# Performance work log

Hardware: AMD Instinct MI355X
Metric: run time of the kernel (lower is better)

The kernel has to match this reference:

```python
import jax, jax.numpy as jnp
import numpy as np

BSZ, SEQ, HID = 4, 2048, 2048
NH, NKV, HD = 16, 8, 128
SLOTS, MAXSEQ = 8, 4096
EPS = 1e-6
SCALE = HD ** -0.5


def rms_norm(x, w):
    # normalize over last dim (head_dim)
    var = jnp.mean(jnp.square(x), axis=-1, keepdims=True)
    return x * jax.lax.rsqrt(var + EPS) * w


def setup_inputs() -> dict:
    key = jax.random.key(0)
    ks = jax.random.split(key, 6)
    return {
        "hidden_states": jax.random.normal(ks[0], (BSZ, SEQ, HID), jnp.float32),
        "positions": jnp.tile(jnp.arange(SEQ, dtype=jnp.int32)[None, :], (BSZ, 1)),
        "k_cache": jnp.zeros((SLOTS, MAXSEQ, NKV, HD), jnp.float32),
        "v_cache": jnp.zeros((SLOTS, MAXSEQ, NKV, HD), jnp.float32),
        "slot_mapping": jnp.arange(BSZ, dtype=jnp.int32),
        "kv_start_indices": jnp.zeros((BSZ,), jnp.int32),
        "seq_lens": jnp.full((BSZ,), SEQ, jnp.int32),
        "qkv_w": jax.random.normal(ks[1], ((NH + 2 * NKV) * HD, HID), jnp.float32) * 0.02,
        "qkv_b": jax.random.normal(ks[2], ((NH + 2 * NKV) * HD,), jnp.float32) * 0.02,
        "o_w": jax.random.normal(ks[3], (HID, NH * HD), jnp.float32) * 0.02,
        "q_norm_w": jnp.ones((HD,), jnp.float32),
        "k_norm_w": jnp.ones((HD,), jnp.float32),
    }


def reference(hidden_states, positions, k_cache, v_cache, slot_mapping,
              kv_start_indices, seq_lens, qkv_w, qkv_b, o_w, q_norm_w, k_norm_w):
    bsz, seq_len, _ = hidden_states.shape
    qkv = jnp.einsum("bsh,oh->bso", hidden_states, qkv_w) + qkv_b
    q, k, v = jnp.split(qkv, [NH * HD, NH * HD + NKV * HD], axis=-1)
    q = rms_norm(q.reshape(bsz, seq_len, NH, HD), q_norm_w)
    k = rms_norm(k.reshape(bsz, seq_len, NKV, HD), k_norm_w)
    v = v.reshape(bsz, seq_len, NKV, HD)

    # paged KV cache scatter: cache[slot, start:start+seq] = k/v  (vectorized over batch)
    rows = kv_start_indices[:, None] + jnp.arange(seq_len)[None, :]  # [B,S]
    k_cache = k_cache.at[slot_mapping[:, None], rows].set(k)
    v_cache = v_cache.at[slot_mapping[:, None], rows].set(v)

    # prefill path (seq_len > 1): gather back up to max_l (= seq_len here, static)
    max_l = seq_len
    k_h = k_cache[slot_mapping, :max_l].transpose(0, 2, 1, 3)  # [B,Hkv,L,D]
    v_h = v_cache[slot_mapping, :max_l].transpose(0, 2, 1, 3)
    n_rep = NH // NKV
    if n_rep > 1:  # repeat_interleave over head dim (GQA)
        k_h = jnp.repeat(k_h, n_rep, axis=1)
        v_h = jnp.repeat(v_h, n_rep, axis=1)

    qh = q.transpose(0, 2, 1, 3)  # [B,H,S,D]
    scores = jnp.einsum("bhqd,bhkd->bhqk", qh, k_h) * SCALE
    causal = jnp.tril(jnp.ones((seq_len, max_l), bool))
    scores = jnp.where(causal[None, None], scores, -jnp.inf)
    attn = jax.nn.softmax(scores, axis=-1)
    out = jnp.einsum("bhqk,bhkd->bhqd", attn, v_h)
    out = out.transpose(0, 2, 1, 3).reshape(bsz, seq_len, NH * HD)
    return jnp.einsum("bso,ho->bsh", out, o_w)
```

## Files before the change

### kernel.cpp

```cpp
#include <hip/hip_runtime.h>
#include <hip/hip_bf16.h>
#include <stdint.h>

typedef unsigned short u16;
typedef __attribute__((ext_vector_type(8))) __bf16 bf16x8;
typedef __attribute__((ext_vector_type(4))) float f32x4;

#define EPSF 1e-6f
#define SCALE 0.08838834764831845f

__device__ __forceinline__ u16 f2bf(float f) {
    union { float f; uint32_t u; } a; a.f = f;
    uint32_t r = a.u + 0x7FFFu + ((a.u >> 16) & 1u);
    return (u16)(r >> 16);
}
__device__ __forceinline__ float bf2f(u16 u) {
    union { uint32_t u; float f; } a; a.u = ((uint32_t)u) << 16;
    return a.f;
}
__device__ __forceinline__ u16 f2bf_n(float f) {
    __hip_bfloat16 h = __float2bfloat16(f);
    return *reinterpret_cast<u16*>(&h);
}

__global__ __launch_bounds__(256) void cvt_all_k(
    const float* __restrict__ a,
    const float* __restrict__ b,
    const float* __restrict__ c,
    u16* __restrict__ out)
{
    long i = (long)blockIdx.x * 256 + threadIdx.x;
    const float* src; long off;
    if (i < 4194304L)      { src = a; off = 0; }
    else if (i < 6291456L) { src = b; off = 4194304L; }
    else                   { src = c; off = 6291456L; }
    float4 v = ((const float4*)src)[i - off];
    ushort4 o;
    o.x = f2bf(v.x); o.y = f2bf(v.y); o.z = f2bf(v.z); o.w = f2bf(v.w);
    ((ushort4*)out)[i] = o;
}

__device__ __forceinline__ void gload16(const u16* g, u16* l) {
    __builtin_amdgcn_global_load_lds(
        (const __attribute__((address_space(1))) uint32_t*)g,
        (__attribute__((address_space(3))) uint32_t*)l, 16, 0, 0);
}

__global__ __launch_bounds__(512, 2) void gemm8_nt(
    const u16* __restrict__ A, const u16* __restrict__ B,
    const float* __restrict__ bias,
    float* __restrict__ Cf, u16* __restrict__ Cb,
    int M, int N, int K)
{
    __shared__ u16 As[2][256 * 64];
    __shared__ u16 Bs[2][256 * 64];

    const int t = threadIdx.x;
    const int lane = t & 63;
    const int g = lane >> 4, lr = lane & 15;
    const int w = t >> 6;
    const int wm = w >> 2, wn = w & 3;

    const int nwg = gridDim.x * gridDim.y;
    const int bid0 = blockIdx.y * gridDim.x + blockIdx.x;
    const int cpx = nwg >> 3;
    const int bids = (bid0 & 7) * cpx + (bid0 >> 3);
    const int bn = (bids % gridDim.x) * 256;
    const int bm = (bids / gridDim.x) * 256;
    const int NT = K >> 6;

    f32x4 z = {0.f, 0.f, 0.f, 0.f};
    f32x4 acc[8][4];
#pragma unroll
    for (int m = 0; m < 8; ++m)
#pragma unroll
        for (int n = 0; n < 4; ++n) acc[m][n] = z;

    auto STAGE2 = [&](int buf, int k0, int p) {
#pragma unroll
        for (int j = 0; j < 2; ++j) {
            int idx = p * 1024 + j * 512 + t;
            int ci = idx & 2047;
            int row = ci >> 3, slot = ci & 7;
            int csrc = slot ^ (row & 7);
            if (idx < 2048)
                gload16(A + (size_t)(bm + row) * K + k0 + csrc * 8, &As[buf][0] + ci * 8);
            else
                gload16(B + (size_t)(bn + row) * K + k0 + csrc * 8, &Bs[buf][0] + ci * 8);
        }
    };

    bf16x8 afr0[4][2], afr1[4][2];
    bf16x8 bf0[2][2], bf1[2][2];

#pragma unroll
    for (int p = 0; p < 4; ++p) STAGE2(0, 0, p);

    for (int kt = 0; kt < NT; ++kt) {
        const int cur = kt & 1;
        const int k0n = (kt + 1) << 6;
        const bool last = (kt == NT - 1);
        const char* Ab = (const char*)&As[cur][0];
        const char* Bb = (const char*)&Bs[cur][0];
        const int swz = (lr & 7) << 4;

        auto LDA = [&](bf16x8 (&dst)[4][2], int mbase) {
#pragma unroll
            for (int mi = 0; mi < 4; ++mi) {
                int row = wm * 128 + (mbase + mi) * 16 + lr;
#pragma unroll
                for (int kc = 0; kc < 2; ++kc)
                    dst[mi][kc] = *(const bf16x8*)(Ab + row * 128 + ((kc * 64 + g * 16) ^ swz));
            }
        };
        auto LDB = [&](bf16x8 (&dst)[2][2], int nbase) {
#pragma unroll
            for (int ni = 0; ni < 2; ++ni) {
                int row = wn * 64 + (nbase + ni) * 16 + lr;
#pragma unroll
                for (int kc = 0; kc < 2; ++kc)
                    dst[ni][kc] = *(const bf16x8*)(Bb + row * 128 + ((kc * 64 + g * 16) ^ swz));
            }
        };
        auto MMA = [&](bf16x8 (&amf)[4][2], int mf0, int nf0, bf16x8 (&bfr)[2][2]) {
            __builtin_amdgcn_s_setprio(1);
#pragma unroll
            for (int mi = 0; mi < 4; ++mi)
#pragma unroll
                for (int ni = 0; ni < 2; ++ni)
#pragma unroll
                    for (int kc = 0; kc < 2; ++kc)
                        acc[mf0 + mi][nf0 + ni] = __builtin_amdgcn_mfma_f32_16x16x32_bf16(
                            amf[mi][kc], bfr[ni][kc], acc[mf0 + mi][nf0 + ni], 0, 0, 0);
            __builtin_amdgcn_s_setprio(0);
        };

        if (!last) {
#pragma unroll
            for (int p = 0; p < 4; ++p) STAGE2(cur ^ 1, k0n, p);
            asm volatile("s_waitcnt vmcnt(8)" ::: "memory");
        } else {
            asm volatile("s_waitcnt vmcnt(0)" ::: "memory");
        }
        __builtin_amdgcn_s_barrier();
        __builtin_amdgcn_sched_barrier(0);

        LDA(afr0, 0); LDB(bf0, 0); LDB(bf1, 2);
        MMA(afr0, 0, 0, bf0);
        MMA(afr0, 0, 2, bf1);
        LDA(afr1, 4);
        MMA(afr1, 4, 2, bf1);
        MMA(afr1, 4, 0, bf0);

        __builtin_amdgcn_sched_barrier(0);
        __builtin_amdgcn_s_barrier();
    }

#pragma unroll
    for (int mf = 0; mf < 8; ++mf) {
#pragma unroll
        for (int nf = 0; nf < 4; ++nf) {
            int col = bn + wn * 64 + nf * 16 + lr;
            float bv = bias ? bias[col] : 0.f;
#pragma unroll
            for (int r = 0; r < 4; ++r) {
                int row = bm + wm * 128 + mf * 16 + g * 4 + r;
                float v = acc[mf][nf][r] + bv;
                if (Cf) Cf[(size_t)row * N + col] = v;
                else    Cb[(size_t)row * N + col] = f2bf(v);
            }
        }
    }
}

__global__ __launch_bounds__(256) void prep_k(
    u16* __restrict__ qkv, const float* __restrict__ qw, const float* __restrict__ kw,
    u16* __restrict__ vt)
{
    __shared__ u16 T[64 * 64];
    const int bid = blockIdx.x;
    const int t = threadIdx.x;

    if (bid < 8192) {
        const int row = bid;
        const int w = t >> 6, l = t & 63;
#pragma unroll
        for (int i = 0; i < 6; ++i) {
            int head = w + i * 4;
            const float* wt = (head < 16) ? qw : kw;
            u16* p = qkv + (size_t)row * 4096 + head * 128;
            uint32_t u = *(const uint32_t*)(p + l * 2);
            float x0 = bf2f((u16)(u & 0xFFFF));
            float x1 = bf2f((u16)(u >> 16));
            float ss = x0 * x0 + x1 * x1;
#pragma unroll
            for (int m = 1; m < 64; m <<= 1) ss += __shfl_xor(ss, m, 64);
            float inv = rsqrtf(ss * (1.0f / 128.0f) + EPSF);
            float r0 = x0 * inv * wt[l * 2];
            float r1 = x1 * inv * wt[l * 2 + 1];
            uint32_t o = (uint32_t)f2bf(r0) | ((uint32_t)f2bf(r1) << 16);
            *(uint32_t*)(p + l * 2) = o;
        }
    } else {
        const int q = bid - 8192;
        const int sx = (q & 31) * 64;
        const int dy = ((q >> 5) & 1) * 64;
        const int z  = q >> 6;
        const int b = z >> 3, hk = z & 7;
#pragma unroll
        for (int j = 0; j < 2; ++j) {
            int idx = t + j * 256;
            int r = idx >> 3, c8 = (idx & 7) * 8;
            uint4 v = *(const uint4*)(qkv + (size_t)(b * 2048 + sx + r) * 4096 + 3072 + hk * 128 + dy + c8);
            int slot = (c8 >> 3) ^ ((r ^ (r >> 3)) & 7);
            *(uint4*)(&T[r * 64 + slot * 8]) = v;
        }
        __syncthreads();
#pragma unroll
        for (int j = 0; j < 2; ++j) {
            int idx = t + j * 256;
            int rr = idx >> 3, cc8 = (idx & 7) * 8;
            u16 tmp[8];
#pragma unroll
            for (int i = 0; i < 8; ++i) {
                int row = cc8 + i;
                int slot = (rr >> 3) ^ ((row ^ (row >> 3)) & 7);
                tmp[i] = T[row * 64 + slot * 8 + (rr & 7)];
            }
            *(uint4*)(vt + ((size_t)z * 128 + dy + rr) * 2048 + sx + cc8) = *(uint4*)tmp;
        }
    }
}

__global__ __launch_bounds__(256, 2) void attn7_k(
    const u16* __restrict__ qkv, const u16* __restrict__ vt,
    u16* __restrict__ aout)
{
    __shared__ u16 Kt[2][64 * 128];
    __shared__ u16 Vl[2][128 * 64];

    const int t = threadIdx.x;
    const int lane = t & 63;
    const int w = t >> 6;
    const int g = lane >> 4, lr = lane & 15;
    const int pr = blockIdx.x, h = blockIdx.y, b = blockIdx.z;
    const int hk = h >> 1;
    const size_t rowb = (size_t)b * 2048;

    const u16* ksrc = qkv + rowb * 4096 + 2048 + hk * 128;
    const u16* vsrc = vt + (size_t)(b * 8 + hk) * 128 * 2048;

    bf16x8 ones8;
    {
        union { bf16x8 v; u16 e[8]; } on;
#pragma unroll
        for (int j = 0; j < 8; ++j) on.e[j] = 0x3F80;
        ones8 = on.v;
    }

    auto STAGE = [&](int buf, int kvb) {
#pragma unroll
        for (int j = 0; j < 4; ++j) {
            int idx = t + j * 256;
            {
                int row = idx >> 4, slot = idx & 15;
                int csrc = (slot & 8) | ((slot & 7) ^ (row & 7));
                gload16(ksrc + (size_t)(kvb + row) * 4096 + csrc * 8, &Kt[buf][0] + idx * 8);
            }
            {
                int row = idx >> 3, slot = idx & 7;
                int csrc = slot ^ (row & 7);
                gload16(vsrc + (size_t)row * 2048 + kvb + csrc * 8, &Vl[buf][0] + idx * 8);
            }
        }
    };

    for (int sub = 0; sub < 2; ++sub) {
        const int qt = sub ? 15 - pr : pr;
        const int qbase = qt * 128;
        const int nt = 2 * qt + 2;

        bf16x8 qf[2][4];
        {
            const u16* qp = qkv + (rowb + qbase + w * 32 + lr) * 4096 + h * 128;
#pragma unroll
            for (int sb = 0; sb < 2; ++sb)
#pragma unroll
                for (int c = 0; c < 4; ++c) {
                    union { bf16x8 v; u16 e[8]; } uq;
                    uq.v = *(const bf16x8*)(qp + sb * 16 * 4096 + c * 32 + g * 8);
#pragma unroll
                    for (int jj = 0; jj < 8; ++jj) uq.e[jj] = f2bf(bf2f(uq.e[jj]) * SCALE);
                    qf[sb][c] = uq.v;
                }
        }

        float m_r2[2];
        f32x4 z = {0.f, 0.f, 0.f, 0.f};
        f32x4 l_acc[2];
        f32x4 o_acc[2][8];
#pragma unroll
        for (int sb = 0; sb < 2; ++sb) {
            m_r2[sb] = -INFINITY;
            l_acc[sb] = z;
#pragma unroll
            for (int d = 0; d < 8; ++d) o_acc[sb][d] = z;
        }

        __syncthreads();
        STAGE(0, 0);

        for (int kt = 0; kt < nt; ++kt) {
            const int cur = kt & 1;
            const int kvb = kt * 64;
            asm volatile("s_waitcnt vmcnt(0)" ::: "memory");
            __builtin_amdgcn_s_barrier();
            __builtin_amdgcn_sched_barrier(0);
            if (kt + 1 < nt) STAGE(cur ^ 1, kvb + 64);
            __builtin_amdgcn_sched_barrier(0);

            const u16* Kc = &Kt[cur][0];
            const u16* Vc = &Vl[cur][0];
            const bool active = !(kt == nt - 1 && w < 2);
            const bool near = (kt >= nt - 2);

            if (active) {
                f32x4 st[2][4];
                __builtin_amdgcn_s_setprio(1);
#pragma unroll
                for (int cb = 0; cb < 4; ++cb) {
                    int row = cb * 16 + lr;
                    st[0][cb] = z; st[1][cb] = z;
#pragma unroll
                    for (int c = 0; c < 4; ++c) {
                        int chunk = c * 4 + g;
                        int slot = (chunk & 8) | ((chunk & 7) ^ (row & 7));
                        bf16x8 kf = *(const bf16x8*)(&Kc[row * 128 + slot * 8]);
                        st[0][cb] = __builtin_amdgcn_mfma_f32_16x16x32_bf16(kf, qf[0][c], st[0][cb], 0, 0, 0);
                        st[1][cb] = __builtin_amdgcn_mfma_f32_16x16x32_bf16(kf, qf[1][c], st[1][cb], 0, 0, 0);
                    }
                }
                __builtin_amdgcn_s_setprio(0);

                const int slo = ((g & 1) << 5) + lr;
                const int shi = slo + 16;
                const bool ghx = (g >> 1) & 1;

#pragma unroll
                for (int sb = 0; sb < 2; ++sb) {
                    const int qa = qbase + w * 32 + sb * 16 + lr;
                    if (near) {
#pragma unroll
                        for (int cb = 0; cb < 4; ++cb)
#pragma unroll
                            for (int r = 0; r < 4; ++r)
                                if (kvb + cb * 16 + g * 4 + r > qa) st[sb][cb][r] = -INFINITY;
                    }
                    f32x4 m4;
#pragma unroll
                    for (int e = 0; e < 4; ++e)
                        m4[e] = fmaxf(fmaxf(st[sb][0][e], st[sb][1][e]),
                                      fmaxf(st[sb][2][e], st[sb][3][e]));
                    float mx = fmaxf(fmaxf(m4[0], m4[1]), fmaxf(m4[2], m4[3]));
                    mx = fmaxf(mx, __shfl_xor(mx, 16));
                    mx = fmaxf(mx, __shfl_xor(mx, 32));
                    float mold = m_r2[sb];
                    float mbase;
                    if (__all(mx <= mold + 8.0f)) {
                        mbase = mold;
                    } else {
                        float mnew = fmaxf(mold, mx);
                        float alpha = __expf(mold - mnew);
#pragma unroll
                        for (int r = 0; r < 4; ++r) {
                            float ar = __shfl(alpha, (lane & 48) | (g * 4 + r), 64);
                            l_acc[sb][r] *= ar;
#pragma unroll
                            for (int d = 0; d < 8; ++d) o_acc[sb][d][r] *= ar;
                        }
                        m_r2[sb] = mnew;
                        mbase = mnew;
                    }
                    uint2 pk[4];
#pragma unroll
                    for (int cb = 0; cb < 4; ++cb) {
                        float p0 = __expf(st[sb][cb][0] - mbase);
                        float p1 = __expf(st[sb][cb][1] - mbase);
                        float p2 = __expf(st[sb][cb][2] - mbase);
                        float p3 = __expf(st[sb][cb][3] - mbase);
                        pk[cb].x = (uint32_t)f2bf_n(p0) | ((uint32_t)f2bf_n(p1) << 16);
                        pk[cb].y = (uint32_t)f2bf_n(p2) | ((uint32_t)f2bf_n(p3) << 16);
                    }

#pragma unroll
                    for (int kk = 0; kk < 2; ++kk) {
                        uint32_t e0 = (uint32_t)__shfl((int)pk[kk * 2].x, slo, 64);
                        uint32_t e1 = (uint32_t)__shfl((int)pk[kk * 2].y, slo, 64);
                        uint32_t e2 = (uint32_t)__shfl((int)pk[kk * 2].x, shi, 64);
                        uint32_t e3 = (uint32_t)__shfl((int)pk[kk * 2].y, shi, 64);
                        uint32_t o0 = (uint32_t)__shfl((int)pk[kk * 2 + 1].x, slo, 64);
                        uint32_t o1 = (uint32_t)__shfl((int)pk[kk * 2 + 1].y, slo, 64);
                        uint32_t o2 = (uint32_t)__shfl((int)pk[kk * 2 + 1].x, shi, 64);
                        uint32_t o3 = (uint32_t)__shfl((int)pk[kk * 2 + 1].y, shi, 64);
                        union { uint32_t u[4]; bf16x8 v; } pa;
                        pa.u[0] = ghx ? o0 : e0;
                        pa.u[1] = ghx ? o1 : e1;
                        pa.u[2] = ghx ? o2 : e2;
                        pa.u[3] = ghx ? o3 : e3;
                        __builtin_amdgcn_s_setprio(1);
                        l_acc[sb] = __builtin_amdgcn_mfma_f32_16x16x32_bf16(pa.v, ones8, l_acc[sb], 0, 0, 0);
#pragma unroll
                        for (int d = 0; d < 8; ++d) {
                            int row = d * 16 + lr;
                            int slot = (kk * 4 + g) ^ (row & 7);
                            bf16x8 vf = *(const bf16x8*)(&Vc[row * 64 + slot * 8]);
                            o_acc[sb][d] = __builtin_amdgcn_mfma_f32_16x16x32_bf16(pa.v, vf, o_acc[sb][d], 0, 0, 0);
                        }
                        __builtin_amdgcn_s_setprio(0);
                    }
                }
            }
            __builtin_amdgcn_sched_barrier(0);
        }

#pragma unroll
        for (int sb = 0; sb < 2; ++sb) {
            const int qrow0 = qbase + w * 32 + sb * 16 + g * 4;
#pragma unroll
            for (int r = 0; r < 4; ++r) {
                float inv = 1.0f / l_acc[sb][r];
                u16* op = aout + (rowb + qrow0 + r) * 2048 + h * 128;
#pragma unroll
                for (int d = 0; d < 8; ++d)
                    op[d * 16 + lr] = f2bf_n(o_acc[sb][d][r] * inv);
            }
        }
    }
}

extern "C" void kernel_launch(void* const* d_in, const int* in_sizes, int n_in,
                              void* d_out, int out_size, void* d_ws, size_t ws_size,
                              hipStream_t stream)
{
    const float* hidden = (const float*)d_in[0];
    const float* qkv_w = (const float*)d_in[7];
    const float* qkv_b = (const float*)d_in[8];
    const float* o_w   = (const float*)d_in[9];
    const float* q_nw  = (const float*)d_in[10];
    const float* k_nw  = (const float*)d_in[11];

    char* ws = (char*)d_ws;
    u16* hid_bf  = (u16*)ws; ws += (size_t)8192 * 2048 * 2;
    u16* wqkv_bf = (u16*)ws; ws += (size_t)4096 * 2048 * 2;
    u16* ow_bf   = (u16*)ws; ws += (size_t)2048 * 2048 * 2;
    u16* qkv_bf  = (u16*)ws; ws += (size_t)8192 * 4096 * 2;
    u16* attn_bf = (u16*)ws; ws += (size_t)8192 * 2048 * 2;
    u16* vt_bf   = hid_bf;

    cvt_all_k<<<28672, 256, 0, stream>>>(hidden, qkv_w, o_w, hid_bf);

    gemm8_nt<<<dim3(16, 32), 512, 0, stream>>>(hid_bf, wqkv_bf, qkv_b,
                                               nullptr, qkv_bf, 8192, 4096, 2048);
    prep_k<<<dim3(10240), 256, 0, stream>>>(qkv_bf, q_nw, k_nw, vt_bf);
    attn7_k<<<dim3(8, 16, 4), 256, 0, stream>>>(qkv_bf, vt_bf, attn_bf);
    gemm8_nt<<<dim3(8, 32), 512, 0, stream>>>(attn_bf, ow_bf, nullptr,
                                              (float*)d_out, nullptr, 8192, 2048, 2048);
}
```

Measured before the change: 378.1 us.

## Shrink GEMM block tile to 128x128 with four waves per block

Replaces the 256x256, 8-wave GEMM with a 128x128, 4-wave variant that has half the LDS footprint and a simpler load-then-MMA inner loop. Grids grow fourfold, giving more blocks per CU and finer load balance. In exchange, per-tile data reuse drops, so global and LDS traffic per FLOP rise, and the interleaved fragment-load/MMA schedule is lost.

```diff
diff --git a/kernel.cpp b/kernel.cpp
--- a/kernel.cpp
+++ b/kernel.cpp
@@ -46,55 +46,51 @@
         (__attribute__((address_space(3))) uint32_t*)l, 16, 0, 0);
 }
 
-__global__ __launch_bounds__(512, 2) void gemm8_nt(
+__global__ __launch_bounds__(256, 2) void gemm4_nt(
     const u16* __restrict__ A, const u16* __restrict__ B,
     const float* __restrict__ bias,
     float* __restrict__ Cf, u16* __restrict__ Cb,
     int M, int N, int K)
 {
-    __shared__ u16 As[2][256 * 64];
-    __shared__ u16 Bs[2][256 * 64];
+    __shared__ u16 As[2][128 * 64];
+    __shared__ u16 Bs[2][128 * 64];
 
     const int t = threadIdx.x;
     const int lane = t & 63;
     const int g = lane >> 4, lr = lane & 15;
     const int w = t >> 6;
-    const int wm = w >> 2, wn = w & 3;
+    const int wm = w >> 1, wn = w & 1;
 
     const int nwg = gridDim.x * gridDim.y;
     const int bid0 = blockIdx.y * gridDim.x + blockIdx.x;
     const int cpx = nwg >> 3;
     const int bids = (bid0 & 7) * cpx + (bid0 >> 3);
-    const int bn = (bids % gridDim.x) * 256;
-    const int bm = (bids / gridDim.x) * 256;
+    const int bn = (bids % gridDim.x) * 128;
+    const int bm = (bids / gridDim.x) * 128;
     const int NT = K >> 6;
 
     f32x4 z = {0.f, 0.f, 0.f, 0.f};
-    f32x4 acc[8][4];
-#pragma unroll
-    for (int m = 0; m < 8; ++m)
+    f32x4 acc[4][4];
+#pragma unroll
+    for (int m = 0; m < 4; ++m)
 #pragma unroll
         for (int n = 0; n < 4; ++n) acc[m][n] = z;
 
-    auto STAGE2 = [&](int buf, int k0, int p) {
-#pragma unroll
-        for (int j = 0; j < 2; ++j) {
-            int idx = p * 1024 + j * 512 + t;
-            int ci = idx & 2047;
+    auto STAGEALL = [&](int buf, int k0) {
+#pragma unroll
+        for (int j = 0; j < 8; ++j) {
+            int idx = j * 256 + t;
+            int ci = idx & 1023;
             int row = ci >> 3, slot = ci & 7;
             int csrc = slot ^ (row & 7);
-            if (idx < 2048)
+            if (idx < 1024)
                 gload16(A + (size_t)(bm + row) * K + k0 + csrc * 8, &As[buf][0] + ci * 8);
             else
                 gload16(B + (size_t)(bn + row) * K + k0 + csrc * 8, &Bs[buf][0] + ci * 8);
         }
     };
 
-    bf16x8 afr0[4][2], afr1[4][2];
-    bf16x8 bf0[2][2], bf1[2][2];
-
-#pragma unroll
-    for (int p = 0; p < 4; ++p) STAGE2(0, 0, p);
+    STAGEALL(0, 0);
 
     for (int kt = 0; kt < NT; ++kt) {
         const int cur = kt & 1;
@@ -104,40 +100,8 @@
         const char* Bb = (const char*)&Bs[cur][0];
         const int swz = (lr & 7) << 4;
 
-        auto LDA = [&](bf16x8 (&dst)[4][2], int mbase) {
-#pragma unroll
-            for (int mi = 0; mi < 4; ++mi) {
-                int row = wm * 128 + (mbase + mi) * 16 + lr;
-#pragma unroll
-                for (int kc = 0; kc < 2; ++kc)
-                    dst[mi][kc] = *(const bf16x8*)(Ab + row * 128 + ((kc * 64 + g * 16) ^ swz));
-            }
-        };
-        auto LDB = [&](bf16x8 (&dst)[2][2], int nbase) {
-#pragma unroll
-            for (int ni = 0; ni < 2; ++ni) {
-                int row = wn * 64 + (nbase + ni) * 16 + lr;
-#pragma unroll
-                for (int kc = 0; kc < 2; ++kc)
-                    dst[ni][kc] = *(const bf16x8*)(Bb + row * 128 + ((kc * 64 + g * 16) ^ swz));
-            }
-        };
-        auto MMA = [&](bf16x8 (&amf)[4][2], int mf0, int nf0, bf16x8 (&bfr)[2][2]) {
-            __builtin_amdgcn_s_setprio(1);
-#pragma unroll
-            for (int mi = 0; mi < 4; ++mi)
-#pragma unroll
-                for (int ni = 0; ni < 2; ++ni)
-#pragma unroll
-                    for (int kc = 0; kc < 2; ++kc)
-                        acc[mf0 + mi][nf0 + ni] = __builtin_amdgcn_mfma_f32_16x16x32_bf16(
-                            amf[mi][kc], bfr[ni][kc], acc[mf0 + mi][nf0 + ni], 0, 0, 0);
-            __builtin_amdgcn_s_setprio(0);
-        };
-
         if (!last) {
-#pragma unroll
-            for (int p = 0; p < 4; ++p) STAGE2(cur ^ 1, k0n, p);
+            STAGEALL(cur ^ 1, k0n);
             asm volatile("s_waitcnt vmcnt(8)" ::: "memory");
         } else {
             asm volatile("s_waitcnt vmcnt(0)" ::: "memory");
@@ -145,26 +109,45 @@
         __builtin_amdgcn_s_barrier();
         __builtin_amdgcn_sched_barrier(0);
 
-        LDA(afr0, 0); LDB(bf0, 0); LDB(bf1, 2);
-        MMA(afr0, 0, 0, bf0);
-        MMA(afr0, 0, 2, bf1);
-        LDA(afr1, 4);
-        MMA(afr1, 4, 2, bf1);
-        MMA(afr1, 4, 0, bf0);
+        bf16x8 afr[4][2], bfr[4][2];
+#pragma unroll
+        for (int mi = 0; mi < 4; ++mi) {
+            int row = wm * 64 + mi * 16 + lr;
+#pragma unroll
+            for (int kc = 0; kc < 2; ++kc)
+                afr[mi][kc] = *(const bf16x8*)(Ab + row * 128 + ((kc * 64 + g * 16) ^ swz));
+        }
+#pragma unroll
+        for (int ni = 0; ni < 4; ++ni) {
+            int row = wn * 64 + ni * 16 + lr;
+#pragma unroll
+            for (int kc = 0; kc < 2; ++kc)
+                bfr[ni][kc] = *(const bf16x8*)(Bb + row * 128 + ((kc * 64 + g * 16) ^ swz));
+        }
+        __builtin_amdgcn_s_setprio(1);
+#pragma unroll
+        for (int mi = 0; mi < 4; ++mi)
+#pragma unroll
+            for (int ni = 0; ni < 4; ++ni)
+#pragma unroll
+                for (int kc = 0; kc < 2; ++kc)
+                    acc[mi][ni] = __builtin_amdgcn_mfma_f32_16x16x32_bf16(
+                        afr[mi][kc], bfr[ni][kc], acc[mi][ni], 0, 0, 0);
+        __builtin_amdgcn_s_setprio(0);
 
         __builtin_amdgcn_sched_barrier(0);
         __builtin_amdgcn_s_barrier();
     }
 
 #pragma unroll
-    for (int mf = 0; mf < 8; ++mf) {
+    for (int mf = 0; mf < 4; ++mf) {
 #pragma unroll
         for (int nf = 0; nf < 4; ++nf) {
             int col = bn + wn * 64 + nf * 16 + lr;
             float bv = bias ? bias[col] : 0.f;
 #pragma unroll
             for (int r = 0; r < 4; ++r) {
-                int row = bm + wm * 128 + mf * 16 + g * 4 + r;
+                int row = bm + wm * 64 + mf * 16 + g * 4 + r;
                 float v = acc[mf][nf][r] + bv;
                 if (Cf) Cf[(size_t)row * N + col] = v;
                 else    Cb[(size_t)row * N + col] = f2bf(v);
@@ -459,10 +442,10 @@
 
     cvt_all_k<<<28672, 256, 0, stream>>>(hidden, qkv_w, o_w, hid_bf);
 
-    gemm8_nt<<<dim3(16, 32), 512, 0, stream>>>(hid_bf, wqkv_bf, qkv_b,
+    gemm4_nt<<<dim3(32, 64), 256, 0, stream>>>(hid_bf, wqkv_bf, qkv_b,
                                                nullptr, qkv_bf, 8192, 4096, 2048);
     prep_k<<<dim3(10240), 256, 0, stream>>>(qkv_bf, q_nw, k_nw, vt_bf);
     attn7_k<<<dim3(8, 16, 4), 256, 0, stream>>>(qkv_bf, vt_bf, attn_bf);
-    gemm8_nt<<<dim3(8, 32), 512, 0, stream>>>(attn_bf, ow_bf, nullptr,
-                                              (float*)d_out, nullptr, 8192, 2048, 2048);
-}
+    gemm4_nt<<<dim3(16, 64), 256, 0, stream>>>(attn_bf, ow_bf, nullptr,
+                                               (float*)d_out, nullptr, 8192, 2048, 2048);
+}
```

New measurement: 408.2 us. 8.0% more time.
